# Kernel tuning notes

Measured on AMD Instinct MI355X. Metric: run time of the kernel, lower is better.

The kernel has to match this reference:

```python
import jax, jax.numpy as jnp
import numpy as np

B, T = 64, 262144

def setup_inputs() -> dict:
    key = jax.random.key(0)
    ks = jax.random.split(key, 6)
    x = jax.random.normal(ks[0], (B, T, 1), dtype=jnp.float32)
    # b's ~ U(-1, 1); a's ~ U(-0.5, 0.5) per DTDFIICell init
    b0 = jax.random.uniform(ks[1], (1,), dtype=jnp.float32, minval=-1.0, maxval=1.0)
    b1 = jax.random.uniform(ks[2], (1,), dtype=jnp.float32, minval=-1.0, maxval=1.0)
    b2 = jax.random.uniform(ks[3], (1,), dtype=jnp.float32, minval=-1.0, maxval=1.0)
    a1 = jax.random.uniform(ks[4], (1,), dtype=jnp.float32, minval=-0.5, maxval=0.5)
    a2 = jax.random.uniform(ks[5], (1,), dtype=jnp.float32, minval=-0.5, maxval=0.5)
    return {"x": x, "b0": b0, "b1": b1, "b2": b2, "a1": a1, "a2": a2}

def reference(x, b0, b1, b2, a1, a2):
    # x: [B, T, 1]; Direct-Form-II biquad recurrence over T.
    batch = x.shape[0]
    xs = jnp.transpose(x[:, :, 0])  # [T, B] time-major for scan

    def step(v, xt):
        # v: [B, 2] delay-line state; xt: [B]
        out = xt * b0 + v[:, 0]
        v_new = jnp.stack(
            [xt * b1 + v[:, 1] - out * a1,
             xt * b2 - out * a2], axis=-1)
        return v_new, out

    v0 = jnp.zeros((batch, 2), dtype=x.dtype)
    _, outs = jax.lax.scan(step, v0, xs)  # outs: [T, B]
    return jnp.transpose(outs)[:, :, None]  # [B, T, 1]
```

## Files before the change

kernel.cpp:

```cpp
#include <hip/hip_runtime.h>


constexpr int BATCH = 64;
constexpr int T_LEN = 262144;
constexpr int TPB   = 256;
constexpr int LPT   = 32;
constexpr int TILE  = TPB * LPT;
constexpr int SPAN  = 2 * TILE;
constexpr int NBPB  = T_LEN / SPAN;
constexpr int NB    = BATCH * NBPB;
constexpr int WUP   = 4096;

typedef float vfloat4 __attribute__((ext_vector_type(4)));

#define MATSQ(m00, m01, m10, m11)                                  \
    {                                                              \
        float n00 = fmaf(m00, m00, m01 * m10);                     \
        float n01 = fmaf(m00, m01, m01 * m11);                     \
        float n10 = fmaf(m10, m00, m11 * m10);                     \
        float n11 = fmaf(m10, m01, m11 * m11);                     \
        m00 = n00; m01 = n01; m10 = n10; m11 = n11;                \
    }

#define CSTEP(p0, p1, xa, xb, xc, xd)                                        \
    {                                                                        \
        float n0 = fmaf(q00, p0, fmaf(q01, p1,                               \
                   fmaf(k3_0, (xa), fmaf(k2_0, (xb),                         \
                   fmaf(k1_0, (xc), c0 * (xd))))));                          \
        float n1 = fmaf(q10, p0, fmaf(q11, p1,                               \
                   fmaf(k3_1, (xa), fmaf(k2_1, (xb),                         \
                   fmaf(k1_1, (xc), c1 * (xd))))));                          \
        p0 = n0; p1 = n1;                                                    \
    }

__global__ __launch_bounds__(TPB, 2) void biquad_2tile(
    const float* __restrict__ x, float* __restrict__ out,
    const float* __restrict__ pb0, const float* __restrict__ pb1,
    const float* __restrict__ pb2, const float* __restrict__ pa1,
    const float* __restrict__ pa2)
{
    __shared__ float ldsA[TPB][LPT + 1];
    __shared__ float ldsB[TPB][LPT + 1];
    __shared__ float swv[24];

    const int tid  = threadIdx.x;
    const int lane = tid & 63;
    const int w    = tid >> 6;
    const int g    = blockIdx.x;
    const int b    = g >> 4;
    const int k    = g & (NBPB - 1);

    const float b0 = *pb0, b1 = *pb1, b2 = *pb2;
    const float a1 = *pa1, a2 = *pa2;
    const float na1 = -a1, na2 = -a2;

    const float c0 = fmaf(na1, b0, b1), c1 = fmaf(na2, b0, b2);
    const float A00 = na1, A01 = 1.f, A10 = na2, A11 = 0.f;
    const float k1_0 = fmaf(A00, c0, A01 * c1);
    const float k1_1 = fmaf(A10, c0, A11 * c1);
    float B00 = A00, B01 = A01, B10 = A10, B11 = A11;
    MATSQ(B00, B01, B10, B11);
    const float k2_0 = fmaf(B00, c0, B01 * c1);
    const float k2_1 = fmaf(B10, c0, B11 * c1);
    const float k3_0 = fmaf(B00, k1_0, B01 * k1_1);
    const float k3_1 = fmaf(B10, k1_0, B11 * k1_1);
    float q00 = B00, q01 = B01, q10 = B10, q11 = B11;
    MATSQ(q00, q01, q10, q11);

    const size_t base = (size_t)b * T_LEN + (size_t)k * SPAN;

    float4 wq[4];
    if (k > 0) {
        const float4* wsrc = reinterpret_cast<const float4*>(x + base - WUP) + tid * 4;
#pragma unroll
        for (int i = 0; i < 4; ++i) wq[i] = wsrc[i];
    }
    const float4* srcA = reinterpret_cast<const float4*>(x + base);
    const float4* srcB = srcA + TILE / 4;

#pragma unroll
    for (int it = 0; it < 8; ++it) {
        int idx = it * TPB + tid;
        float4 v = srcA[idx];
        int e = idx * 4, c = e >> 5, t = e & 31;
        ldsA[c][t] = v.x; ldsA[c][t + 1] = v.y;
        ldsA[c][t + 2] = v.z; ldsA[c][t + 3] = v.w;
    }
#pragma unroll
    for (int it = 0; it < 8; ++it) {
        int idx = it * TPB + tid;
        float4 v = srcB[idx];
        int e = idx * 4, c = e >> 5, t = e & 31;
        ldsB[c][t] = v.x; ldsB[c][t + 1] = v.y;
        ldsB[c][t + 2] = v.z; ldsB[c][t + 3] = v.w;
    }
    __syncthreads();

    float xv[LPT];
#pragma unroll
    for (int t = 0; t < LPT; ++t) xv[t] = ldsA[tid][t];

    float pW0 = 0.f, pW1 = 0.f;
    if (k > 0) {
#pragma unroll
        for (int i = 0; i < 4; ++i)
            CSTEP(pW0, pW1, wq[i].x, wq[i].y, wq[i].z, wq[i].w);
    }
    float pA0 = 0.f, pA1 = 0.f;
#pragma unroll
    for (int i = 0; i < LPT / 4; ++i)
        CSTEP(pA0, pA1, xv[4 * i], xv[4 * i + 1], xv[4 * i + 2], xv[4 * i + 3]);
    float pB0 = 0.f, pB1 = 0.f;
#pragma unroll
    for (int i = 0; i < LPT / 4; ++i)
        CSTEP(pB0, pB1, ldsB[tid][4 * i], ldsB[tid][4 * i + 1],
                        ldsB[tid][4 * i + 2], ldsB[tid][4 * i + 3]);

    float wW00 = q00, wW01 = q01, wW10 = q10, wW11 = q11;
    MATSQ(wW00, wW01, wW10, wW11);
    MATSQ(wW00, wW01, wW10, wW11);
    float m00 = wW00, m01 = wW01, m10 = wW10, m11 = wW11;
    MATSQ(m00, m01, m10, m11);
    float wM00 = m00, wM01 = m01, wM10 = m10, wM11 = m11;

    for (int d = 1; d < 64; d <<= 1) {
        float oW0 = __shfl_up(pW0, d), oW1 = __shfl_up(pW1, d);
        float oA0 = __shfl_up(pA0, d), oA1 = __shfl_up(pA1, d);
        float oB0 = __shfl_up(pB0, d), oB1 = __shfl_up(pB1, d);
        if (lane >= d) {
            pW0 = fmaf(wW00, oW0, fmaf(wW01, oW1, pW0));
            pW1 = fmaf(wW10, oW0, fmaf(wW11, oW1, pW1));
            pA0 = fmaf(wM00, oA0, fmaf(wM01, oA1, pA0));
            pA1 = fmaf(wM10, oA0, fmaf(wM11, oA1, pA1));
            pB0 = fmaf(wM00, oB0, fmaf(wM01, oB1, pB0));
            pB1 = fmaf(wM10, oB0, fmaf(wM11, oB1, pB1));
        }
        MATSQ(wW00, wW01, wW10, wW11);
        MATSQ(wM00, wM01, wM10, wM11);
    }

    float einA0 = __shfl_up(pA0, 1), einA1 = __shfl_up(pA1, 1);
    float einB0 = __shfl_up(pB0, 1), einB1 = __shfl_up(pB1, 1);
    if (lane == 0) { einA0 = einA1 = einB0 = einB1 = 0.f; }

    if (lane == 63) {
        swv[6 * w]     = pW0; swv[6 * w + 1] = pW1;
        swv[6 * w + 2] = pA0; swv[6 * w + 3] = pA1;
        swv[6 * w + 4] = pB0; swv[6 * w + 5] = pB1;
    }
    __syncthreads();

    float sA0 = 0.f, sA1 = 0.f;
#pragma unroll
    for (int u = 0; u < 4; ++u) {
        float t0 = fmaf(wW00, sA0, fmaf(wW01, sA1, swv[6 * u]));
        float t1 = fmaf(wW10, sA0, fmaf(wW11, sA1, swv[6 * u + 1]));
        sA0 = t0; sA1 = t1;
    }
    float agA0 = 0.f, agA1 = 0.f;
#pragma unroll
    for (int u = 0; u < 4; ++u) {
        float t0 = fmaf(wM00, agA0, fmaf(wM01, agA1, swv[6 * u + 2]));
        float t1 = fmaf(wM10, agA0, fmaf(wM11, agA1, swv[6 * u + 3]));
        agA0 = t0; agA1 = t1;
    }
    float cwA0 = 0.f, cwA1 = 0.f, cwB0 = 0.f, cwB1 = 0.f;
    for (int u = 0; u < w; ++u) {
        float t0 = fmaf(wM00, cwA0, fmaf(wM01, cwA1, swv[6 * u + 2]));
        float t1 = fmaf(wM10, cwA0, fmaf(wM11, cwA1, swv[6 * u + 3]));
        cwA0 = t0; cwA1 = t1;
        float u0 = fmaf(wM00, cwB0, fmaf(wM01, cwB1, swv[6 * u + 4]));
        float u1 = fmaf(wM10, cwB0, fmaf(wM11, cwB1, swv[6 * u + 5]));
        cwB0 = u0; cwB1 = u1;
    }
    float P00 = wM00, P01 = wM01, P10 = wM10, P11 = wM11;
    MATSQ(P00, P01, P10, P11);
    MATSQ(P00, P01, P10, P11);
    float sB0 = fmaf(P00, sA0, fmaf(P01, sA1, agA0));
    float sB1 = fmaf(P10, sA0, fmaf(P11, sA1, agA1));

    float vA0 = sA0, vA1 = sA1, vB0 = sB0, vB1 = sB1;
    float vcA0 = cwA0, vcA1 = cwA1, vcB0 = cwB0, vcB1 = cwB1;
    {
        float t00 = m00, t01 = m01, t10 = m10, t11 = m11;
#pragma unroll
        for (int bit = 0; bit < 8; ++bit) {
            if ((tid >> bit) & 1) {
                float n0, n1;
                n0 = fmaf(t00, vA0, t01 * vA1); n1 = fmaf(t10, vA0, t11 * vA1);
                vA0 = n0; vA1 = n1;
                n0 = fmaf(t00, vB0, t01 * vB1); n1 = fmaf(t10, vB0, t11 * vB1);
                vB0 = n0; vB1 = n1;
                if (bit < 6) {
                    n0 = fmaf(t00, vcA0, t01 * vcA1); n1 = fmaf(t10, vcA0, t11 * vcA1);
                    vcA0 = n0; vcA1 = n1;
                    n0 = fmaf(t00, vcB0, t01 * vcB1); n1 = fmaf(t10, vcB0, t11 * vcB1);
                    vcB0 = n0; vcB1 = n1;
                }
            }
            MATSQ(t00, t01, t10, t11);
        }
    }
    float v0 = vA0 + vcA0 + einA0;
    float v1 = vA1 + vcA1 + einA1;
    float u0 = vB0 + vcB0 + einB0;
    float u1 = vB1 + vcB1 + einB1;

    {
        float o2 = fmaf(xv[0], b0, v0);
        float vn0 = fmaf(na1, o2, fmaf(xv[0], b1, v1));
        float o1 = fmaf(xv[1], b0, vn0);
        ldsA[tid][0] = o2; ldsA[tid][1] = o1;
#pragma unroll
        for (int t = 2; t < LPT; ++t) {
            float acc = fmaf(b1, xv[t - 1], fmaf(b2, xv[t - 2], na2 * o2));
            float o   = fmaf(b0, xv[t], fmaf(na1, o1, acc));
            ldsA[tid][t] = o;
            o2 = o1; o1 = o;
        }
    }
    {
        float xm2 = ldsB[tid][0], xm1 = ldsB[tid][1];
        float o2 = fmaf(xm2, b0, u0);
        float vn0 = fmaf(na1, o2, fmaf(xm2, b1, u1));
        float o1 = fmaf(xm1, b0, vn0);
        ldsB[tid][0] = o2; ldsB[tid][1] = o1;
#pragma unroll
        for (int t = 2; t < LPT; ++t) {
            float xt  = ldsB[tid][t];
            float acc = fmaf(b1, xm1, fmaf(b2, xm2, na2 * o2));
            float o   = fmaf(b0, xt, fmaf(na1, o1, acc));
            ldsB[tid][t] = o;
            xm2 = xm1; xm1 = xt;
            o2 = o1; o1 = o;
        }
    }
    __syncthreads();

    vfloat4* dstA = reinterpret_cast<vfloat4*>(out + base);
    vfloat4* dstB = dstA + TILE / 4;
#pragma unroll
    for (int it = 0; it < 8; ++it) {
        int idx = it * TPB + tid;
        int e = idx * 4, c = e >> 5, t = e & 31;
        vfloat4 v;
        v.x = ldsA[c][t];     v.y = ldsA[c][t + 1];
        v.z = ldsA[c][t + 2]; v.w = ldsA[c][t + 3];
        __builtin_nontemporal_store(v, &dstA[idx]);
    }
#pragma unroll
    for (int it = 0; it < 8; ++it) {
        int idx = it * TPB + tid;
        int e = idx * 4, c = e >> 5, t = e & 31;
        vfloat4 v;
        v.x = ldsB[c][t];     v.y = ldsB[c][t + 1];
        v.z = ldsB[c][t + 2]; v.w = ldsB[c][t + 3];
        __builtin_nontemporal_store(v, &dstB[idx]);
    }
}

extern "C" void kernel_launch(void* const* d_in, const int* in_sizes, int n_in,
                              void* d_out, int out_size, void* d_ws, size_t ws_size,
                              hipStream_t stream) {
    const float* x   = (const float*)d_in[0];
    const float* pb0 = (const float*)d_in[1];
    const float* pb1 = (const float*)d_in[2];
    const float* pb2 = (const float*)d_in[3];
    const float* pa1 = (const float*)d_in[4];
    const float* pa2 = (const float*)d_in[5];
    float* out = (float*)d_out;

    biquad_2tile<<<NB, TPB, 0, stream>>>(x, out, pb0, pb1, pb2, pa1, pa2);
}
```

Baseline: 32.02 us.

## Load inputs directly into registers, share one LDS tile, remap blocks across XCDs

Each thread now loads its own contiguous 32-element rows straight from global memory into registers, instead of staging both tiles through LDS with a coalesced transpose. One LDS buffer is reused to transpose outputs for tile A and then tile B, which halves shared memory, and the launch bound is raised to four blocks per CU. Block indices are remapped so neighbouring chunks land on the same XCD. The cost is uncoalesced strided global loads (128 B per thread per row), more register pressure from holding 64 input floats, and two extra barriers.

```diff
diff --git a/kernel.cpp b/kernel.cpp
--- a/kernel.cpp
+++ b/kernel.cpp
@@ -10,6 +10,8 @@
 constexpr int NBPB  = T_LEN / SPAN;
 constexpr int NB    = BATCH * NBPB;
 constexpr int WUP   = 4096;
+constexpr int NXCD  = 8;
+constexpr int CPX   = NB / NXCD;
 
 typedef float vfloat4 __attribute__((ext_vector_type(4)));
 
@@ -33,20 +35,20 @@
         p0 = n0; p1 = n1;                                                    \
     }
 
-__global__ __launch_bounds__(TPB, 2) void biquad_2tile(
+__global__ __launch_bounds__(TPB, 4) void biquad_pair(
     const float* __restrict__ x, float* __restrict__ out,
     const float* __restrict__ pb0, const float* __restrict__ pb1,
     const float* __restrict__ pb2, const float* __restrict__ pa1,
     const float* __restrict__ pa2)
 {
-    __shared__ float ldsA[TPB][LPT + 1];
-    __shared__ float ldsB[TPB][LPT + 1];
+    __shared__ float lds[TPB][LPT + 1];
     __shared__ float swv[24];
 
     const int tid  = threadIdx.x;
     const int lane = tid & 63;
     const int w    = tid >> 6;
-    const int g    = blockIdx.x;
+
+    const int g    = (blockIdx.x & (NXCD - 1)) * CPX + (blockIdx.x >> 3);
     const int b    = g >> 4;
     const int k    = g & (NBPB - 1);
 
@@ -71,34 +73,18 @@
 
     float4 wq[4];
     if (k > 0) {
-        const float4* wsrc = reinterpret_cast<const float4*>(x + base - WUP) + tid * 4;
+        const float4* wsrc =
+            reinterpret_cast<const float4*>(x + base - WUP) + tid * 4;
 #pragma unroll
         for (int i = 0; i < 4; ++i) wq[i] = wsrc[i];
     }
-    const float4* srcA = reinterpret_cast<const float4*>(x + base);
-    const float4* srcB = srcA + TILE / 4;
-
-#pragma unroll
-    for (int it = 0; it < 8; ++it) {
-        int idx = it * TPB + tid;
-        float4 v = srcA[idx];
-        int e = idx * 4, c = e >> 5, t = e & 31;
-        ldsA[c][t] = v.x; ldsA[c][t + 1] = v.y;
-        ldsA[c][t + 2] = v.z; ldsA[c][t + 3] = v.w;
-    }
-#pragma unroll
-    for (int it = 0; it < 8; ++it) {
-        int idx = it * TPB + tid;
-        float4 v = srcB[idx];
-        int e = idx * 4, c = e >> 5, t = e & 31;
-        ldsB[c][t] = v.x; ldsB[c][t + 1] = v.y;
-        ldsB[c][t + 2] = v.z; ldsB[c][t + 3] = v.w;
-    }
-    __syncthreads();
-
-    float xv[LPT];
-#pragma unroll
-    for (int t = 0; t < LPT; ++t) xv[t] = ldsA[tid][t];
+    const float4* xrowA = reinterpret_cast<const float4*>(x + base) + tid * (LPT / 4);
+    const float4* xrowB = xrowA + TILE / 4;
+    float4 xqA[8], xqB[8];
+#pragma unroll
+    for (int i = 0; i < 8; ++i) xqA[i] = xrowA[i];
+#pragma unroll
+    for (int i = 0; i < 8; ++i) xqB[i] = xrowB[i];
 
     float pW0 = 0.f, pW1 = 0.f;
     if (k > 0) {
@@ -108,35 +94,34 @@
     }
     float pA0 = 0.f, pA1 = 0.f;
 #pragma unroll
-    for (int i = 0; i < LPT / 4; ++i)
-        CSTEP(pA0, pA1, xv[4 * i], xv[4 * i + 1], xv[4 * i + 2], xv[4 * i + 3]);
+    for (int i = 0; i < 8; ++i)
+        CSTEP(pA0, pA1, xqA[i].x, xqA[i].y, xqA[i].z, xqA[i].w);
     float pB0 = 0.f, pB1 = 0.f;
 #pragma unroll
-    for (int i = 0; i < LPT / 4; ++i)
-        CSTEP(pB0, pB1, ldsB[tid][4 * i], ldsB[tid][4 * i + 1],
-                        ldsB[tid][4 * i + 2], ldsB[tid][4 * i + 3]);
-
-    float wW00 = q00, wW01 = q01, wW10 = q10, wW11 = q11;
-    MATSQ(wW00, wW01, wW10, wW11);
-    MATSQ(wW00, wW01, wW10, wW11);
-    float m00 = wW00, m01 = wW01, m10 = wW10, m11 = wW11;
+    for (int i = 0; i < 8; ++i)
+        CSTEP(pB0, pB1, xqB[i].x, xqB[i].y, xqB[i].z, xqB[i].w);
+
+    float wa00 = q00, wa01 = q01, wa10 = q10, wa11 = q11;
+    MATSQ(wa00, wa01, wa10, wa11);
+    MATSQ(wa00, wa01, wa10, wa11);
+    float m00 = wa00, m01 = wa01, m10 = wa10, m11 = wa11;
     MATSQ(m00, m01, m10, m11);
-    float wM00 = m00, wM01 = m01, wM10 = m10, wM11 = m11;
+    float wb00 = m00, wb01 = m01, wb10 = m10, wb11 = m11;
 
     for (int d = 1; d < 64; d <<= 1) {
         float oW0 = __shfl_up(pW0, d), oW1 = __shfl_up(pW1, d);
         float oA0 = __shfl_up(pA0, d), oA1 = __shfl_up(pA1, d);
         float oB0 = __shfl_up(pB0, d), oB1 = __shfl_up(pB1, d);
         if (lane >= d) {
-            pW0 = fmaf(wW00, oW0, fmaf(wW01, oW1, pW0));
-            pW1 = fmaf(wW10, oW0, fmaf(wW11, oW1, pW1));
-            pA0 = fmaf(wM00, oA0, fmaf(wM01, oA1, pA0));
-            pA1 = fmaf(wM10, oA0, fmaf(wM11, oA1, pA1));
-            pB0 = fmaf(wM00, oB0, fmaf(wM01, oB1, pB0));
-            pB1 = fmaf(wM10, oB0, fmaf(wM11, oB1, pB1));
-        }
-        MATSQ(wW00, wW01, wW10, wW11);
-        MATSQ(wM00, wM01, wM10, wM11);
+            pW0 = fmaf(wa00, oW0, fmaf(wa01, oW1, pW0));
+            pW1 = fmaf(wa10, oW0, fmaf(wa11, oW1, pW1));
+            pA0 = fmaf(wb00, oA0, fmaf(wb01, oA1, pA0));
+            pA1 = fmaf(wb10, oA0, fmaf(wb11, oA1, pA1));
+            pB0 = fmaf(wb00, oB0, fmaf(wb01, oB1, pB0));
+            pB1 = fmaf(wb10, oB0, fmaf(wb11, oB1, pB1));
+        }
+        MATSQ(wa00, wa01, wa10, wa11);
+        MATSQ(wb00, wb01, wb10, wb11);
     }
 
     float einA0 = __shfl_up(pA0, 1), einA1 = __shfl_up(pA1, 1);
@@ -153,27 +138,27 @@
     float sA0 = 0.f, sA1 = 0.f;
 #pragma unroll
     for (int u = 0; u < 4; ++u) {
-        float t0 = fmaf(wW00, sA0, fmaf(wW01, sA1, swv[6 * u]));
-        float t1 = fmaf(wW10, sA0, fmaf(wW11, sA1, swv[6 * u + 1]));
+        float t0 = fmaf(wa00, sA0, fmaf(wa01, sA1, swv[6 * u]));
+        float t1 = fmaf(wa10, sA0, fmaf(wa11, sA1, swv[6 * u + 1]));
         sA0 = t0; sA1 = t1;
     }
     float agA0 = 0.f, agA1 = 0.f;
 #pragma unroll
     for (int u = 0; u < 4; ++u) {
-        float t0 = fmaf(wM00, agA0, fmaf(wM01, agA1, swv[6 * u + 2]));
-        float t1 = fmaf(wM10, agA0, fmaf(wM11, agA1, swv[6 * u + 3]));
+        float t0 = fmaf(wb00, agA0, fmaf(wb01, agA1, swv[6 * u + 2]));
+        float t1 = fmaf(wb10, agA0, fmaf(wb11, agA1, swv[6 * u + 3]));
         agA0 = t0; agA1 = t1;
     }
     float cwA0 = 0.f, cwA1 = 0.f, cwB0 = 0.f, cwB1 = 0.f;
     for (int u = 0; u < w; ++u) {
-        float t0 = fmaf(wM00, cwA0, fmaf(wM01, cwA1, swv[6 * u + 2]));
-        float t1 = fmaf(wM10, cwA0, fmaf(wM11, cwA1, swv[6 * u + 3]));
+        float t0 = fmaf(wb00, cwA0, fmaf(wb01, cwA1, swv[6 * u + 2]));
+        float t1 = fmaf(wb10, cwA0, fmaf(wb11, cwA1, swv[6 * u + 3]));
         cwA0 = t0; cwA1 = t1;
-        float u0 = fmaf(wM00, cwB0, fmaf(wM01, cwB1, swv[6 * u + 4]));
-        float u1 = fmaf(wM10, cwB0, fmaf(wM11, cwB1, swv[6 * u + 5]));
+        float u0 = fmaf(wb00, cwB0, fmaf(wb01, cwB1, swv[6 * u + 4]));
+        float u1 = fmaf(wb10, cwB0, fmaf(wb11, cwB1, swv[6 * u + 5]));
         cwB0 = u0; cwB1 = u1;
     }
-    float P00 = wM00, P01 = wM01, P10 = wM10, P11 = wM11;
+    float P00 = wb00, P01 = wb01, P10 = wb10, P11 = wb11;
     MATSQ(P00, P01, P10, P11);
     MATSQ(P00, P01, P10, P11);
     float sB0 = fmaf(P00, sA0, fmaf(P01, sA1, agA0));
@@ -201,36 +186,25 @@
             MATSQ(t00, t01, t10, t11);
         }
     }
-    float v0 = vA0 + vcA0 + einA0;
-    float v1 = vA1 + vcA1 + einA1;
-    float u0 = vB0 + vcB0 + einB0;
-    float u1 = vB1 + vcB1 + einB1;
+    const float vAs0 = vA0 + vcA0 + einA0;
+    const float vAs1 = vA1 + vcA1 + einA1;
+    const float vBs0 = vB0 + vcB0 + einB0;
+    const float vBs1 = vB1 + vcB1 + einB1;
 
     {
-        float o2 = fmaf(xv[0], b0, v0);
-        float vn0 = fmaf(na1, o2, fmaf(xv[0], b1, v1));
-        float o1 = fmaf(xv[1], b0, vn0);
-        ldsA[tid][0] = o2; ldsA[tid][1] = o1;
+        float xm2 = xqA[0].x, xm1 = xqA[0].y;
+        float o2 = fmaf(xm2, b0, vAs0);
+        float vn0 = fmaf(na1, o2, fmaf(xm2, b1, vAs1));
+        float o1 = fmaf(xm1, b0, vn0);
+        lds[tid][0] = o2; lds[tid][1] = o1;
 #pragma unroll
         for (int t = 2; t < LPT; ++t) {
-            float acc = fmaf(b1, xv[t - 1], fmaf(b2, xv[t - 2], na2 * o2));
-            float o   = fmaf(b0, xv[t], fmaf(na1, o1, acc));
-            ldsA[tid][t] = o;
-            o2 = o1; o1 = o;
-        }
-    }
-    {
-        float xm2 = ldsB[tid][0], xm1 = ldsB[tid][1];
-        float o2 = fmaf(xm2, b0, u0);
-        float vn0 = fmaf(na1, o2, fmaf(xm2, b1, u1));
-        float o1 = fmaf(xm1, b0, vn0);
-        ldsB[tid][0] = o2; ldsB[tid][1] = o1;
-#pragma unroll
-        for (int t = 2; t < LPT; ++t) {
-            float xt  = ldsB[tid][t];
+            float xt = (t & 3) == 0 ? xqA[t >> 2].x :
+                       (t & 3) == 1 ? xqA[t >> 2].y :
+                       (t & 3) == 2 ? xqA[t >> 2].z : xqA[t >> 2].w;
             float acc = fmaf(b1, xm1, fmaf(b2, xm2, na2 * o2));
             float o   = fmaf(b0, xt, fmaf(na1, o1, acc));
-            ldsB[tid][t] = o;
+            lds[tid][t] = o;
             xm2 = xm1; xm1 = xt;
             o2 = o1; o1 = o;
         }
@@ -238,23 +212,45 @@
     __syncthreads();
 
     vfloat4* dstA = reinterpret_cast<vfloat4*>(out + base);
-    vfloat4* dstB = dstA + TILE / 4;
 #pragma unroll
     for (int it = 0; it < 8; ++it) {
         int idx = it * TPB + tid;
         int e = idx * 4, c = e >> 5, t = e & 31;
         vfloat4 v;
-        v.x = ldsA[c][t];     v.y = ldsA[c][t + 1];
-        v.z = ldsA[c][t + 2]; v.w = ldsA[c][t + 3];
+        v.x = lds[c][t];     v.y = lds[c][t + 1];
+        v.z = lds[c][t + 2]; v.w = lds[c][t + 3];
         __builtin_nontemporal_store(v, &dstA[idx]);
     }
+    __syncthreads();
+
+    {
+        float xm2 = xqB[0].x, xm1 = xqB[0].y;
+        float o2 = fmaf(xm2, b0, vBs0);
+        float vn0 = fmaf(na1, o2, fmaf(xm2, b1, vBs1));
+        float o1 = fmaf(xm1, b0, vn0);
+        lds[tid][0] = o2; lds[tid][1] = o1;
+#pragma unroll
+        for (int t = 2; t < LPT; ++t) {
+            float xt = (t & 3) == 0 ? xqB[t >> 2].x :
+                       (t & 3) == 1 ? xqB[t >> 2].y :
+                       (t & 3) == 2 ? xqB[t >> 2].z : xqB[t >> 2].w;
+            float acc = fmaf(b1, xm1, fmaf(b2, xm2, na2 * o2));
+            float o   = fmaf(b0, xt, fmaf(na1, o1, acc));
+            lds[tid][t] = o;
+            xm2 = xm1; xm1 = xt;
+            o2 = o1; o1 = o;
+        }
+    }
+    __syncthreads();
+
+    vfloat4* dstB = dstA + TILE / 4;
 #pragma unroll
     for (int it = 0; it < 8; ++it) {
         int idx = it * TPB + tid;
         int e = idx * 4, c = e >> 5, t = e & 31;
         vfloat4 v;
-        v.x = ldsB[c][t];     v.y = ldsB[c][t + 1];
-        v.z = ldsB[c][t + 2]; v.w = ldsB[c][t + 3];
+        v.x = lds[c][t];     v.y = lds[c][t + 1];
+        v.z = lds[c][t + 2]; v.w = lds[c][t + 3];
         __builtin_nontemporal_store(v, &dstB[idx]);
     }
 }
@@ -270,5 +266,5 @@
     const float* pa2 = (const float*)d_in[5];
     float* out = (float*)d_out;
 
-    biquad_2tile<<<NB, TPB, 0, stream>>>(x, out, pb0, pb1, pb2, pa1, pa2);
+    biquad_pair<<<NB, TPB, 0, stream>>>(x, out, pb0, pb1, pb2, pa1, pa2);
 }
```

Result: slower. 35.60 us (+11.2%).
